# Kernel tuning notes

Measured on AMD Instinct MI355X. Metric: run time of the kernel, lower is better.

The kernel has to match this reference:

```python
import jax, jax.numpy as jnp
import numpy as np

DEPTH, HEADS, DIM_HEAD, DIM, MLP, PATCH_DIM, NP_, NC = 8, 8, 64, 512, 2048, 512, 1024, 2
INNER = HEADS * DIM_HEAD
SCALE = DIM_HEAD ** -0.5
EPS = 1e-5

def layernorm(x, s, b):
    m = x.mean(-1, keepdims=True)
    v = ((x - m) ** 2).mean(-1, keepdims=True)
    return (x - m) * jax.lax.rsqrt(v + EPS) * s + b

def setup_inputs() -> dict:
    key = jax.random.key(0)
    ks = jax.random.split(key, 24)
    g = lambda k, sh, sc=0.02: jax.random.normal(k, sh, dtype=jnp.float32) * sc
    return {
        "img": jax.random.normal(ks[0], (4, NP_, PATCH_DIM), dtype=jnp.float32),
        "embed_w": g(ks[1], (PATCH_DIM, DIM)), "embed_b": jnp.zeros((DIM,), jnp.float32),
        "pos_emb": g(ks[2], (1, NP_ + 1, DIM), 1.0), "cls_token": g(ks[3], (1, 1, DIM), 1.0),
        "ln1_s": jnp.ones((DEPTH, DIM), jnp.float32), "ln1_b": jnp.zeros((DEPTH, DIM), jnp.float32),
        "qkv_w": g(ks[4], (DEPTH, DIM, 3 * INNER)),
        "out_w": g(ks[5], (DEPTH, INNER, DIM)), "out_b": jnp.zeros((DEPTH, DIM), jnp.float32),
        "ln2_s": jnp.ones((DEPTH, DIM), jnp.float32), "ln2_b": jnp.zeros((DEPTH, DIM), jnp.float32),
        "ff_w1": g(ks[6], (DEPTH, DIM, MLP)), "ff_b1": jnp.zeros((DEPTH, MLP), jnp.float32),
        "ff_w2": g(ks[7], (DEPTH, MLP, DIM)), "ff_b2": jnp.zeros((DEPTH, DIM), jnp.float32),
        "head_ln_s": jnp.ones((DIM,), jnp.float32), "head_ln_b": jnp.zeros((DIM,), jnp.float32),
        "head_w": g(ks[8], (DIM, NC)), "head_b": jnp.zeros((NC,), jnp.float32),
    }

def reference(img, embed_w, embed_b, pos_emb, cls_token, ln1_s, ln1_b, qkv_w, out_w, out_b,
              ln2_s, ln2_b, ff_w1, ff_b1, ff_w2, ff_b2, head_ln_s, head_ln_b, head_w, head_b):
    B, N, _ = img.shape
    x = img @ embed_w + embed_b                       # [B, N, DIM]
    cls = jnp.broadcast_to(cls_token, (B, 1, DIM))
    x = jnp.concatenate([cls, x], axis=1) + pos_emb[:, :N + 1]
    for l in range(DEPTH):
        h = layernorm(x, ln1_s[l], ln1_b[l])
        qkv = h @ qkv_w[l]                            # [B, N+1, 3*INNER]
        q, k, v = jnp.split(qkv, 3, axis=-1)
        rh = lambda t: t.reshape(B, N + 1, HEADS, DIM_HEAD).transpose(0, 2, 1, 3)
        q, k, v = rh(q), rh(k), rh(v)                 # [B, H, N+1, Dh]
        dots = jnp.einsum('bhnd,bhmd->bhnm', q, k) * SCALE
        attn = jax.nn.softmax(dots, axis=-1)
        o = jnp.einsum('bhnm,bhmd->bhnd', attn, v)
        o = o.transpose(0, 2, 1, 3).reshape(B, N + 1, INNER)
        x = o @ out_w[l] + out_b[l] + x
        h = layernorm(x, ln2_s[l], ln2_b[l])
        h = jax.nn.gelu(h @ ff_w1[l] + ff_b1[l], approximate=False)
        x = h @ ff_w2[l] + ff_b2[l] + x
    x = x[:, 0]                                       # cls pooling
    x = layernorm(x, head_ln_s, head_ln_b)
    return (jax.nn.sigmoid(x @ head_w + head_b),)
```

## Files before the change

### kernel.cpp

```cpp
#include <hip/hip_runtime.h>
#include <math.h>
#include <stdint.h>

#define NHEADS   8
#define DHEAD    64
#define DIMM     512
#define MLPD     2048
#define NPATCH   1024
#define NTOK     1025
#define BATCH    4
#define ROWS     (BATCH*NTOK)
#define TOKPAD   1088
#define NCHUNK   17
#define CSPLIT   9
#define QSC      0.180336881f
#define LN_EPS   1e-5f

typedef __attribute__((ext_vector_type(8))) short short8;
typedef __attribute__((ext_vector_type(4))) float f32x4;

__device__ __forceinline__ unsigned short f2bf(float f) {
  union { float f; unsigned u; } c; c.f = f;
  unsigned u = c.u;
  return (unsigned short)((u + 0x7fffu + ((u >> 16) & 1u)) >> 16);
}
__device__ __forceinline__ unsigned short f2bf_fast(float f) {
  union { float f; unsigned u; } c; c.f = f;
  return (unsigned short)((c.u + 0x8000u) >> 16);
}
__device__ __forceinline__ float bf2f(unsigned short b) {
  union { unsigned u; float f; } c; c.u = (unsigned)b << 16;
  return c.f;
}

__device__ __forceinline__ float wsum(float v) {
#pragma unroll
  for (int o = 32; o > 0; o >>= 1) v += __shfl_xor(v, o, 64);
  return v;
}

__device__ __forceinline__ void gl_lds16(const void* g, const void* l) {
  __builtin_amdgcn_global_load_lds(
      (const __attribute__((address_space(1))) unsigned int*)(uintptr_t)g,
      (__attribute__((address_space(3))) unsigned int*)(unsigned int)(uintptr_t)l,
      16, 0, 0);
}

template <int TM, int TN, int WR, int WC, bool ACOMB>
__global__ __launch_bounds__(256) void mgemm_k(
    const unsigned short* __restrict__ A, const unsigned short* __restrict__ Bt,
    const float* __restrict__ bias, const float* __restrict__ res,
    void* __restrict__ Cout, int M, int N, int K, int flags,
    unsigned short* __restrict__ vTout, const float* __restrict__ mlc,
    const float* __restrict__ posp)
{
  constexpr int AF = TM / WR / 16;
  constexpr int BF = TN / WC / 16;
  constexpr int AG = TM / 32;
  constexpr int BG = TN / 32;
  __shared__ unsigned short sA[2][TM * 64];
  __shared__ unsigned short sB[2][TN * 64];
  const int tid = threadIdx.x;
  const int w = tid >> 6, lane = tid & 63;
  const int quad = lane >> 4, l15 = lane & 15;
  const int m0 = blockIdx.y * TM, n0 = blockIdx.x * TN;
  const int wrow = (w / WC) * (TM / WR);
  const int wcol = (w % WC) * (TN / WC);
  const int lrow = lane >> 3;
  const int lkg = (lane & 7) ^ lrow;

  size_t abase[AG], bbase[BG];
  int arow[AG];
#pragma unroll
  for (int g = 0; g < AG; g++) {
    int grp = w * AG + g;
    int ar = m0 + grp * 8 + lrow; ar = ar < M ? ar : M - 1;
    arow[g] = ar;
    abase[g] = (size_t)ar * K + lkg * 8;
  }
#pragma unroll
  for (int g = 0; g < BG; g++) {
    int grp = w * BG + g;
    int br = n0 + grp * 8 + lrow;
    bbase[g] = (size_t)br * K + lkg * 8;
  }

  auto stageB = [&](int k0, int buf) {
#pragma unroll
    for (int g = 0; g < BG; g++)
      gl_lds16(Bt + bbase[g] + k0, &sB[buf][(w * BG + g) * 512]);
  };
  auto stageA_dma = [&](int k0, int buf) {
#pragma unroll
    for (int g = 0; g < AG; g++)
      gl_lds16(A + abase[g] + k0, &sA[buf][(w * AG + g) * 512]);
  };

  uint4 ra0[AG], ra1[AG];
  float rl0[AG], rl1[AG];
  auto loadAC = [&](int k0) {
    const int h = k0 >> 6;
#pragma unroll
    for (int g = 0; g < AG; g++) {
      size_t off = abase[g] + k0;
      ra0[g] = *(const uint4*)(A + off);
      ra1[g] = *(const uint4*)(A + (size_t)ROWS * DIMM + off);
      int b = arow[g] / NTOK, tok = arow[g] - b * NTOK;
      int bh = b * 8 + h;
      rl0[g] = mlc[(size_t)bh * NTOK + tok];
      rl1[g] = mlc[(size_t)(32 + bh) * NTOK + tok];
    }
  };
  auto writeAC = [&](int buf) {
#pragma unroll
    for (int g = 0; g < AG; g++) {
      float inv = 1.0f / (rl0[g] + rl1[g]);
      const unsigned short* p0 = (const unsigned short*)&ra0[g];
      const unsigned short* p1 = (const unsigned short*)&ra1[g];
      alignas(16) unsigned short o[8];
#pragma unroll
      for (int i = 0; i < 8; i++)
        o[i] = f2bf((bf2f(p0[i]) + bf2f(p1[i])) * inv);
      *(uint4*)&sA[buf][(w * AG + g) * 512 + lane * 8] = *(const uint4*)o;
    }
  };

  f32x4 acc[AF][BF];
#pragma unroll
  for (int i = 0; i < AF; i++)
#pragma unroll
    for (int j = 0; j < BF; j++) { f32x4 z = {0.f, 0.f, 0.f, 0.f}; acc[i][j] = z; }

  if (ACOMB) { stageB(0, 0); loadAC(0); writeAC(0); }
  else       { stageA_dma(0, 0); stageB(0, 0); }

  const int nsteps = K >> 6;
  for (int step = 0; step < nsteps; step++) {
    const int buf = step & 1;
    __syncthreads();
    if (step + 1 < nsteps) {
      stageB((step + 1) << 6, buf ^ 1);
      if (ACOMB) loadAC((step + 1) << 6);
      else       stageA_dma((step + 1) << 6, buf ^ 1);
    }
#pragma unroll
    for (int kk = 0; kk < 2; kk++) {
      short8 af[AF], bfr[BF];
#pragma unroll
      for (int i = 0; i < AF; i++) {
        int r = wrow + i * 16 + l15;
        af[i] = *(const short8*)&sA[buf][r * 64 + (((kk * 4 + quad) ^ (lane & 7)) << 3)];
      }
#pragma unroll
      for (int j = 0; j < BF; j++) {
        int r = wcol + j * 16 + l15;
        bfr[j] = *(const short8*)&sB[buf][r * 64 + (((kk * 4 + quad) ^ (lane & 7)) << 3)];
      }
#pragma unroll
      for (int i = 0; i < AF; i++)
#pragma unroll
        for (int j = 0; j < BF; j++)
          acc[i][j] = __builtin_amdgcn_mfma_f32_16x16x32_bf16(af[i], bfr[j], acc[i][j], 0, 0, 0);
    }
    if (ACOMB && step + 1 < nsteps) writeAC(buf ^ 1);
  }

  const bool do_gelu = flags & 1;
  const bool out_bf  = flags & 2;
  const bool embedf  = flags & 4;
#pragma unroll
  for (int i = 0; i < AF; i++) {
#pragma unroll
    for (int j = 0; j < BF; j++) {
      const int col = n0 + wcol + j * 16 + l15;
      const bool vcol = (vTout != nullptr) && (col >= 1024);
      alignas(8) unsigned short vb[4];
#pragma unroll
      for (int rg = 0; rg < 4; rg++) {
        int row = m0 + wrow + i * 16 + quad * 4 + rg;
        if (row >= M) continue;
        float v = acc[i][j][rg];
        if (bias) v += bias[col];
        if (do_gelu) v = 0.5f * v * (1.0f + erff(v * 0.70710678118654752f));
        if (res) v += res[(size_t)row * N + col];
        if (embedf) {
          int bb = row >> 10, t = (row & 1023) + 1;
          ((float*)Cout)[((size_t)(bb * NTOK + t)) * N + col] =
              v + posp[(size_t)t * N + col];
        } else if (out_bf) {
          unsigned short bv = f2bf(v);
          vb[rg] = bv;
          if (!vcol) ((unsigned short*)Cout)[(size_t)row * N + col] = bv;
        } else {
          ((float*)Cout)[(size_t)row * N + col] = v;
        }
      }
      if (vcol) {
        const int hcol = col - 1024, h = hcol >> 6, d = hcol & 63;
#pragma unroll
        for (int rg = 0; rg < 4; rg++) {
          int row = m0 + wrow + i * 16 + quad * 4 + rg;
          if (row >= M) continue;
          int bb = row / NTOK, tok = row - bb * NTOK;
          vTout[((size_t)(bb * 8 + h) * 64 + d) * TOKPAD + tok] = vb[rg];
        }
      }
    }
  }
}

__global__ __launch_bounds__(256) void attn_k(
    const unsigned short* __restrict__ qkv, const unsigned short* __restrict__ vT,
    unsigned short* __restrict__ po, float* __restrict__ ml)
{
  __shared__ unsigned short ps[64 * 64];
  __shared__ unsigned short ks[2][64 * 64];
  __shared__ unsigned short vs[2][64 * 64];
  const int bid = blockIdx.x;
  const int g8 = bid & 7, ii = bid >> 3;
  const int bh = (g8 << 2) | (ii & 3);
  const int rest = ii >> 2;
  const int q0 = (rest % 17) * 64;
  const int split = rest / 17;
  const int b = bh >> 3, h = bh & 7;
  const int tid = threadIdx.x, w = tid >> 6, lane = tid & 63;
  const int quad = lane >> 4, l15 = lane & 15;
  const int lrow = lane >> 3, lkg = (lane & 7) ^ lrow;
  const unsigned short* qbase = qkv + (size_t)(b * NTOK) * 1536 + h * 64;
  const unsigned short* kbase = qbase + 512;
  const unsigned short* vtb   = vT + (size_t)bh * 64 * TOKPAD;

  auto stage_kv = [&](int c0, int buf) {
#pragma unroll
    for (int g = 0; g < 2; g++) {
      int grp = w * 2 + g;
      int tok = c0 + grp * 8 + lrow; tok = tok < NTOK ? tok : NTOK - 1;
      gl_lds16(kbase + (size_t)tok * 1536 + lkg * 8, &ks[buf][grp * 512]);
      int d = grp * 8 + lrow;
      gl_lds16(vtb + (size_t)d * TOKPAD + c0 + lkg * 8, &vs[buf][grp * 512]);
    }
  };

  const int cbeg = split ? CSPLIT : 0;
  const int cend = split ? NCHUNK : CSPLIT;
  stage_kv(cbeg * 64, 0);

  int qr = q0 + w * 16 + l15; qr = qr < NTOK ? qr : NTOK - 1;
  const unsigned short* qrow = qbase + (size_t)qr * 1536;
  short8 aq[2];
  aq[0] = *(const short8*)(qrow + quad * 8);
  aq[1] = *(const short8*)(qrow + 32 + quad * 8);
#pragma unroll
  for (int k = 0; k < 2; k++)
#pragma unroll
    for (int i = 0; i < 8; i++)
      aq[k][i] = (short)f2bf(bf2f((unsigned short)aq[k][i]) * QSC);

  short8 ones;
#pragma unroll
  for (int i = 0; i < 8; i++) ones[i] = (short)0x3F80;

  f32x4 Oa[4];
#pragma unroll
  for (int n = 0; n < 4; n++) { f32x4 z = {0.f, 0.f, 0.f, 0.f}; Oa[n] = z; }
  float lst[4] = {0.f, 0.f, 0.f, 0.f};

  for (int c = cbeg; c < cend; c++) {
    const int c0 = c * 64;
    const int buf = (c - cbeg) & 1;
    __syncthreads();
    if (c + 1 < cend) stage_kv(c0 + 64, buf ^ 1);

    f32x4 sa[4];
#pragma unroll
    for (int n = 0; n < 4; n++) {
      f32x4 s = {0.f, 0.f, 0.f, 0.f};
#pragma unroll
      for (int kk = 0; kk < 2; kk++) {
        short8 bk = *(const short8*)&ks[buf][(n * 16 + l15) * 64 + (((kk * 4 + quad) ^ (lane & 7)) << 3)];
        s = __builtin_amdgcn_mfma_f32_16x16x32_bf16(aq[kk], bk, s, 0, 0, 0);
      }
      sa[n] = s;
    }

    if (c0 + 64 > NTOK) {
#pragma unroll
      for (int n = 0; n < 4; n++) {
        bool oob = (c0 + n * 16 + l15) >= NTOK;
#pragma unroll
        for (int rg = 0; rg < 4; rg++)
          if (oob) sa[n][rg] = -1e30f;
      }
    }

#pragma unroll
    for (int n = 0; n < 4; n++)
#pragma unroll
      for (int rg = 0; rg < 4; rg++) {
        int row = w * 16 + quad * 4 + rg;
        int key = n * 16 + l15;
        ps[row * 64 + ((((key >> 3) ^ (row & 7)) & 7) << 3) + (key & 7)] =
            f2bf_fast(exp2f(sa[n][rg]));
      }

    short8 ap[2];
#pragma unroll
    for (int kk = 0; kk < 2; kk++)
      ap[kk] = *(const short8*)&ps[(w * 16 + l15) * 64 + (((kk * 4 + quad) ^ (lane & 7)) << 3)];

    f32x4 lsum = {0.f, 0.f, 0.f, 0.f};
#pragma unroll
    for (int kk = 0; kk < 2; kk++)
      lsum = __builtin_amdgcn_mfma_f32_16x16x32_bf16(ap[kk], ones, lsum, 0, 0, 0);
#pragma unroll
    for (int rg = 0; rg < 4; rg++) lst[rg] += lsum[rg];

#pragma unroll
    for (int n = 0; n < 4; n++) {
      f32x4 o = Oa[n];
#pragma unroll
      for (int kk = 0; kk < 2; kk++) {
        short8 bv = *(const short8*)&vs[buf][(n * 16 + l15) * 64 + (((kk * 4 + quad) ^ (lane & 7)) << 3)];
        o = __builtin_amdgcn_mfma_f32_16x16x32_bf16(ap[kk], bv, o, 0, 0, 0);
      }
      Oa[n] = o;
    }
  }

  unsigned short* pob = po + (size_t)split * ROWS * DIMM;
#pragma unroll
  for (int n = 0; n < 4; n++)
#pragma unroll
    for (int rg = 0; rg < 4; rg++) {
      int tok = q0 + w * 16 + quad * 4 + rg;
      if (tok < NTOK)
        pob[(size_t)(b * NTOK + tok) * DIMM + h * 64 + n * 16 + l15] = f2bf(Oa[n][rg]);
    }
  if (l15 == 0) {
#pragma unroll
    for (int rg = 0; rg < 4; rg++) {
      int tok = q0 + w * 16 + quad * 4 + rg;
      if (tok < NTOK)
        ml[(size_t)(split * 32 + bh) * NTOK + tok] = lst[rg];
    }
  }
}

__global__ __launch_bounds__(256) void ln_k(
    const float* __restrict__ X, const float* __restrict__ s,
    const float* __restrict__ b, unsigned short* __restrict__ Y, int nrows)
{
  const int w = threadIdx.x >> 6, lane = threadIdx.x & 63;
  const int row = blockIdx.x * 4 + w;
  if (row >= nrows) return;
  const float* x = X + (size_t)row * DIMM;
  float4 v0 = *(const float4*)(x + lane * 8);
  float4 v1 = *(const float4*)(x + lane * 8 + 4);
  float xv[8] = {v0.x, v0.y, v0.z, v0.w, v1.x, v1.y, v1.z, v1.w};
  float sum = 0.f, sq = 0.f;
#pragma unroll
  for (int i = 0; i < 8; i++) { sum += xv[i]; sq += xv[i] * xv[i]; }
  sum = wsum(sum); sq = wsum(sq);
  const float mean = sum * (1.0f / DIMM);
  const float var  = sq * (1.0f / DIMM) - mean * mean;
  const float r    = rsqrtf(var + LN_EPS);
  alignas(16) unsigned short tmp[8];
#pragma unroll
  for (int i = 0; i < 8; i++) {
    int d = lane * 8 + i;
    tmp[i] = f2bf((xv[i] - mean) * r * s[d] + b[d]);
  }
  *(uint4*)&Y[(size_t)row * DIMM + lane * 8] = *(const uint4*)tmp;
}

#define CLS_B   8
#define IMG_B   2048
#define TC0     (CLS_B + IMG_B)
#define TQKV    (TC0 + 64)
#define TOUT    (TQKV + 1536)
#define TFF1    (TOUT + 512)
#define TFF2    (TFF1 + 2048)
#define TEND    (TFF2 + 2048)

__global__ __launch_bounds__(256) void prep_k(
    const float* __restrict__ embed_w, const float* __restrict__ qkv_w,
    const float* __restrict__ out_w, const float* __restrict__ ff1_w,
    const float* __restrict__ ff2_w,
    unsigned short* __restrict__ wt_embed, unsigned short* __restrict__ wt_qkv,
    unsigned short* __restrict__ wt_out, unsigned short* __restrict__ wt_ff1,
    unsigned short* __restrict__ wt_ff2,
    const float* __restrict__ img, unsigned short* __restrict__ img_bf,
    const float* __restrict__ cls, const float* __restrict__ pos,
    float* __restrict__ x)
{
  __shared__ float tl[32][129];
  const int bid = blockIdx.x, tid = threadIdx.x;
  if (bid < CLS_B) {
    int idx = bid * 256 + tid;
    int b = idx >> 9, d = idx & 511;
    x[(size_t)b * NTOK * DIMM + d] = cls[d] + pos[d];
    return;
  }
  if (bid < TC0) {
    int i = (bid - CLS_B) * 256 + tid;
    float4 v = ((const float4*)img)[i];
    alignas(8) unsigned short o[4] = {f2bf(v.x), f2bf(v.y), f2bf(v.z), f2bf(v.w)};
    ((uint2*)img_bf)[i] = *(const uint2*)o;
    return;
  }
  const float* W; unsigned short* Wt; int K, N, t;
  if (bid < TQKV)      { W = embed_w; Wt = wt_embed; K = 512;  N = 512;  t = bid - TC0;  }
  else if (bid < TOUT) { W = qkv_w;   Wt = wt_qkv;   K = 512;  N = 1536; t = bid - TQKV; }
  else if (bid < TFF1) { W = out_w;   Wt = wt_out;   K = 512;  N = 512;  t = bid - TOUT; }
  else if (bid < TFF2) { W = ff1_w;   Wt = wt_ff1;   K = 512;  N = 2048; t = bid - TFF1; }
  else                 { W = ff2_w;   Wt = wt_ff2;   K = 2048; N = 512;  t = bid - TFF2; }
  const int ntx = N >> 5;
  const int tpz = ntx * (K >> 7);
  const int z = t / tpz, r = t - z * tpz;
  const int n0 = (r % ntx) << 5, k0 = (r / ntx) << 7;
  const size_t off = (size_t)z * K * N;
  const float* Wz = W + off;
  unsigned short* Wtz = Wt + off;
#pragma unroll
  for (int it = 0; it < 4; it++) {
    int lin = it * 256 + tid;
    int k = lin >> 3, f4 = (lin & 7) << 2;
    float4 v = *(const float4*)&Wz[(size_t)(k0 + k) * N + n0 + f4];
    tl[f4 + 0][k] = v.x; tl[f4 + 1][k] = v.y;
    tl[f4 + 2][k] = v.z; tl[f4 + 3][k] = v.w;
  }
  __syncthreads();
  const int n = tid >> 3, kg = tid & 7;
#pragma unroll
  for (int j = 0; j < 2; j++) {
    int kb = kg * 16 + j * 8;
    alignas(16) unsigned short o[8];
#pragma unroll
    for (int i = 0; i < 8; i++) o[i] = f2bf(tl[n][kb + i]);
    *(uint4*)&Wtz[(size_t)(n0 + n) * K + k0 + kb] = *(const uint4*)o;
  }
}

__global__ __launch_bounds__(256) void head_k(
    const float* __restrict__ X, const float* __restrict__ s,
    const float* __restrict__ bln, const float* __restrict__ W,
    const float* __restrict__ bh, float* __restrict__ out)
{
  const int w = threadIdx.x >> 6, lane = threadIdx.x & 63;
  if (w >= BATCH) return;
  const float* x = X + (size_t)w * NTOK * DIMM;
  float4 v0 = *(const float4*)(x + lane * 8);
  float4 v1 = *(const float4*)(x + lane * 8 + 4);
  float xv[8] = {v0.x, v0.y, v0.z, v0.w, v1.x, v1.y, v1.z, v1.w};
  float sum = 0.f, sq = 0.f;
#pragma unroll
  for (int i = 0; i < 8; i++) { sum += xv[i]; sq += xv[i] * xv[i]; }
  sum = wsum(sum); sq = wsum(sq);
  const float mean = sum * (1.0f / DIMM);
  const float var  = sq * (1.0f / DIMM) - mean * mean;
  const float r    = rsqrtf(var + LN_EPS);
  float l0 = 0.f, l1 = 0.f;
#pragma unroll
  for (int i = 0; i < 8; i++) {
    int d = lane * 8 + i;
    float xn = (xv[i] - mean) * r * s[d] + bln[d];
    l0 = fmaf(xn, W[d * 2 + 0], l0);
    l1 = fmaf(xn, W[d * 2 + 1], l1);
  }
  l0 = wsum(l0); l1 = wsum(l1);
  if (lane == 0) {
    out[w * 2 + 0] = 1.0f / (1.0f + expf(-(l0 + bh[0])));
    out[w * 2 + 1] = 1.0f / (1.0f + expf(-(l1 + bh[1])));
  }
}

extern "C" void kernel_launch(void* const* d_in, const int* in_sizes, int n_in,
                              void* d_out, int out_size, void* d_ws, size_t ws_size,
                              hipStream_t stream)
{
  const float* img       = (const float*)d_in[0];
  const float* embed_w   = (const float*)d_in[1];
  const float* embed_b   = (const float*)d_in[2];
  const float* pos_emb   = (const float*)d_in[3];
  const float* cls_token = (const float*)d_in[4];
  const float* ln1_s     = (const float*)d_in[5];
  const float* ln1_b     = (const float*)d_in[6];
  const float* qkv_w     = (const float*)d_in[7];
  const float* out_w     = (const float*)d_in[8];
  const float* out_b     = (const float*)d_in[9];
  const float* ln2_s     = (const float*)d_in[10];
  const float* ln2_b     = (const float*)d_in[11];
  const float* ff_w1     = (const float*)d_in[12];
  const float* ff_b1     = (const float*)d_in[13];
  const float* ff_w2     = (const float*)d_in[14];
  const float* ff_b2     = (const float*)d_in[15];
  const float* head_ln_s = (const float*)d_in[16];
  const float* head_ln_b = (const float*)d_in[17];
  const float* head_w    = (const float*)d_in[18];
  const float* head_b    = (const float*)d_in[19];
  float* out = (float*)d_out;

  char* p = (char*)d_ws;
  auto alloc = [&](size_t bytes) { char* r = p; p += (bytes + 255) & ~(size_t)255; return r; };

  unsigned short* wt_embed = (unsigned short*)alloc((size_t)512 * 512 * 2);
  unsigned short* wt_qkv   = (unsigned short*)alloc((size_t)8 * 1536 * 512 * 2);
  unsigned short* wt_out   = (unsigned short*)alloc((size_t)8 * 512 * 512 * 2);
  unsigned short* wt_ff1   = (unsigned short*)alloc((size_t)8 * 2048 * 512 * 2);
  unsigned short* wt_ff2   = (unsigned short*)alloc((size_t)8 * 512 * 2048 * 2);
  unsigned short* img_bf   = (unsigned short*)alloc((size_t)4096 * 512 * 2);
  float*          x        = (float*)alloc((size_t)ROWS * DIMM * 4);
  unsigned short* h        = (unsigned short*)alloc((size_t)ROWS * DIMM * 2);
  unsigned short* vTb      = (unsigned short*)alloc((size_t)32 * 64 * TOKPAD * 2);
  unsigned short* po       = (unsigned short*)alloc((size_t)2 * ROWS * DIMM * 2);
  float*          mlb      = (float*)alloc((size_t)2 * 32 * NTOK * 4);
  char*           big      = alloc((size_t)ROWS * MLPD * 2);
  unsigned short* qkvb     = (unsigned short*)big;
  unsigned short* ffh      = (unsigned short*)big;

  dim3 blk(256);

  prep_k<<<TEND, blk, 0, stream>>>(
      embed_w, qkv_w, out_w, ff_w1, ff_w2,
      wt_embed, wt_qkv, wt_out, wt_ff1, wt_ff2,
      img, img_bf, cls_token, pos_emb, x);

  mgemm_k<32, 64, 2, 2, false><<<dim3(8, 128), blk, 0, stream>>>(
      img_bf, wt_embed, embed_b, nullptr, x, 4096, 512, 512, 4,
      nullptr, nullptr, pos_emb);

  const int mt32 = (ROWS + 31) / 32;
  for (int l = 0; l < 8; l++) {
    ln_k<<<(ROWS + 3) / 4, blk, 0, stream>>>(
        x, ln1_s + l * DIMM, ln1_b + l * DIMM, h, ROWS);
    mgemm_k<32, 64, 2, 2, false><<<dim3(24, mt32), blk, 0, stream>>>(
        h, wt_qkv + (size_t)l * 1536 * 512, nullptr, nullptr,
        qkvb, ROWS, 1536, 512, 2, vTb, nullptr, nullptr);
    attn_k<<<dim3(1088), blk, 0, stream>>>(qkvb, vTb, po, mlb);
    mgemm_k<32, 64, 2, 2, true><<<dim3(8, mt32), blk, 0, stream>>>(
        po, wt_out + (size_t)l * 512 * 512, out_b + l * DIMM, x,
        x, ROWS, 512, 512, 0, nullptr, mlb, nullptr);
    ln_k<<<(ROWS + 3) / 4, blk, 0, stream>>>(
        x, ln2_s + l * DIMM, ln2_b + l * DIMM, h, ROWS);
    mgemm_k<32, 64, 2, 2, false><<<dim3(32, mt32), blk, 0, stream>>>(
        h, wt_ff1 + (size_t)l * 2048 * 512, ff_b1 + l * MLPD, nullptr,
        ffh, ROWS, 2048, 512, 1 | 2, nullptr, nullptr, nullptr);
    mgemm_k<32, 64, 2, 2, false><<<dim3(8, mt32), blk, 0, stream>>>(
        ffh, wt_ff2 + (size_t)l * 512 * 2048, ff_b2 + l * DIMM, x,
        x, ROWS, 512, 2048, 0, nullptr, nullptr, nullptr);
  }

  head_k<<<1, blk, 0, stream>>>(x, head_ln_s, head_ln_b, head_w, head_b, out);
}
```

Baseline: 1.190 ms.

## Process 128 query rows per attention block to reuse staged K/V tiles

Each attention block now covers 128 query rows instead of 64. Each wave handles two 16-row query groups against the same K/V chunk already staged in shared memory, and the grid shrinks from 1088 to 576 blocks. This halves the global-to-LDS K/V traffic and staging per query row. In exchange each wave holds twice as many accumulator registers, and there are fewer blocks to spread across the CUs, which may hurt occupancy and load balance.

```diff
diff --git a/kernel.cpp b/kernel.cpp
--- a/kernel.cpp
+++ b/kernel.cpp
@@ -220,8 +220,8 @@
   const int g8 = bid & 7, ii = bid >> 3;
   const int bh = (g8 << 2) | (ii & 3);
   const int rest = ii >> 2;
-  const int q0 = (rest % 17) * 64;
-  const int split = rest / 17;
+  const int q0 = (rest % 9) * 128;
+  const int split = rest / 9;
   const int b = bh >> 3, h = bh & 7;
   const int tid = threadIdx.x, w = tid >> 6, lane = tid & 63;
   const int quad = lane >> 4, l15 = lane & 15;
@@ -245,25 +245,30 @@
   const int cend = split ? NCHUNK : CSPLIT;
   stage_kv(cbeg * 64, 0);
 
-  int qr = q0 + w * 16 + l15; qr = qr < NTOK ? qr : NTOK - 1;
-  const unsigned short* qrow = qbase + (size_t)qr * 1536;
-  short8 aq[2];
-  aq[0] = *(const short8*)(qrow + quad * 8);
-  aq[1] = *(const short8*)(qrow + 32 + quad * 8);
-#pragma unroll
-  for (int k = 0; k < 2; k++)
-#pragma unroll
-    for (int i = 0; i < 8; i++)
-      aq[k][i] = (short)f2bf(bf2f((unsigned short)aq[k][i]) * QSC);
+  short8 aq[2][2];
+#pragma unroll
+  for (int g16 = 0; g16 < 2; g16++) {
+    int qr = q0 + w * 32 + g16 * 16 + l15; qr = qr < NTOK ? qr : NTOK - 1;
+    const unsigned short* qrow = qbase + (size_t)qr * 1536;
+    aq[g16][0] = *(const short8*)(qrow + quad * 8);
+    aq[g16][1] = *(const short8*)(qrow + 32 + quad * 8);
+#pragma unroll
+    for (int k = 0; k < 2; k++)
+#pragma unroll
+      for (int i = 0; i < 8; i++)
+        aq[g16][k][i] = (short)f2bf(bf2f((unsigned short)aq[g16][k][i]) * QSC);
+  }
 
   short8 ones;
 #pragma unroll
   for (int i = 0; i < 8; i++) ones[i] = (short)0x3F80;
 
-  f32x4 Oa[4];
-#pragma unroll
-  for (int n = 0; n < 4; n++) { f32x4 z = {0.f, 0.f, 0.f, 0.f}; Oa[n] = z; }
-  float lst[4] = {0.f, 0.f, 0.f, 0.f};
+  f32x4 Oa[2][4];
+#pragma unroll
+  for (int g16 = 0; g16 < 2; g16++)
+#pragma unroll
+    for (int n = 0; n < 4; n++) { f32x4 z = {0.f, 0.f, 0.f, 0.f}; Oa[g16][n] = z; }
+  float lst[2][4] = {{0.f, 0.f, 0.f, 0.f}, {0.f, 0.f, 0.f, 0.f}};
 
   for (int c = cbeg; c < cend; c++) {
     const int c0 = c * 64;
@@ -271,77 +276,83 @@
     __syncthreads();
     if (c + 1 < cend) stage_kv(c0 + 64, buf ^ 1);
 
-    f32x4 sa[4];
-#pragma unroll
-    for (int n = 0; n < 4; n++) {
-      f32x4 s = {0.f, 0.f, 0.f, 0.f};
-#pragma unroll
-      for (int kk = 0; kk < 2; kk++) {
-        short8 bk = *(const short8*)&ks[buf][(n * 16 + l15) * 64 + (((kk * 4 + quad) ^ (lane & 7)) << 3)];
-        s = __builtin_amdgcn_mfma_f32_16x16x32_bf16(aq[kk], bk, s, 0, 0, 0);
-      }
-      sa[n] = s;
-    }
-
-    if (c0 + 64 > NTOK) {
+#pragma unroll
+    for (int g16 = 0; g16 < 2; g16++) {
+      f32x4 sa[4];
 #pragma unroll
       for (int n = 0; n < 4; n++) {
-        bool oob = (c0 + n * 16 + l15) >= NTOK;
-#pragma unroll
-        for (int rg = 0; rg < 4; rg++)
-          if (oob) sa[n][rg] = -1e30f;
-      }
-    }
-
+        f32x4 s = {0.f, 0.f, 0.f, 0.f};
+#pragma unroll
+        for (int kk = 0; kk < 2; kk++) {
+          short8 bk = *(const short8*)&ks[buf][(n * 16 + l15) * 64 + (((kk * 4 + quad) ^ (lane & 7)) << 3)];
+          s = __builtin_amdgcn_mfma_f32_16x16x32_bf16(aq[g16][kk], bk, s, 0, 0, 0);
+        }
+        sa[n] = s;
+      }
+
+      if (c0 + 64 > NTOK) {
+#pragma unroll
+        for (int n = 0; n < 4; n++) {
+          bool oob = (c0 + n * 16 + l15) >= NTOK;
+#pragma unroll
+          for (int rg = 0; rg < 4; rg++)
+            if (oob) sa[n][rg] = -1e30f;
+        }
+      }
+
+#pragma unroll
+      for (int n = 0; n < 4; n++)
+#pragma unroll
+        for (int rg = 0; rg < 4; rg++) {
+          int row = w * 16 + quad * 4 + rg;
+          int key = n * 16 + l15;
+          ps[row * 64 + ((((key >> 3) ^ (row & 7)) & 7) << 3) + (key & 7)] =
+              f2bf_fast(exp2f(sa[n][rg]));
+        }
+
+      short8 ap[2];
+#pragma unroll
+      for (int kk = 0; kk < 2; kk++)
+        ap[kk] = *(const short8*)&ps[(w * 16 + l15) * 64 + (((kk * 4 + quad) ^ (lane & 7)) << 3)];
+
+      f32x4 lsum = {0.f, 0.f, 0.f, 0.f};
+#pragma unroll
+      for (int kk = 0; kk < 2; kk++)
+        lsum = __builtin_amdgcn_mfma_f32_16x16x32_bf16(ap[kk], ones, lsum, 0, 0, 0);
+#pragma unroll
+      for (int rg = 0; rg < 4; rg++) lst[g16][rg] += lsum[rg];
+
+#pragma unroll
+      for (int n = 0; n < 4; n++) {
+        f32x4 o = Oa[g16][n];
+#pragma unroll
+        for (int kk = 0; kk < 2; kk++) {
+          short8 bv = *(const short8*)&vs[buf][(n * 16 + l15) * 64 + (((kk * 4 + quad) ^ (lane & 7)) << 3)];
+          o = __builtin_amdgcn_mfma_f32_16x16x32_bf16(ap[kk], bv, o, 0, 0, 0);
+        }
+        Oa[g16][n] = o;
+      }
+    }
+  }
+
+  unsigned short* pob = po + (size_t)split * ROWS * DIMM;
+#pragma unroll
+  for (int g16 = 0; g16 < 2; g16++) {
 #pragma unroll
     for (int n = 0; n < 4; n++)
 #pragma unroll
       for (int rg = 0; rg < 4; rg++) {
-        int row = w * 16 + quad * 4 + rg;
-        int key = n * 16 + l15;
-        ps[row * 64 + ((((key >> 3) ^ (row & 7)) & 7) << 3) + (key & 7)] =
-            f2bf_fast(exp2f(sa[n][rg]));
-      }
-
-    short8 ap[2];
-#pragma unroll
-    for (int kk = 0; kk < 2; kk++)
-      ap[kk] = *(const short8*)&ps[(w * 16 + l15) * 64 + (((kk * 4 + quad) ^ (lane & 7)) << 3)];
-
-    f32x4 lsum = {0.f, 0.f, 0.f, 0.f};
-#pragma unroll
-    for (int kk = 0; kk < 2; kk++)
-      lsum = __builtin_amdgcn_mfma_f32_16x16x32_bf16(ap[kk], ones, lsum, 0, 0, 0);
-#pragma unroll
-    for (int rg = 0; rg < 4; rg++) lst[rg] += lsum[rg];
-
-#pragma unroll
-    for (int n = 0; n < 4; n++) {
-      f32x4 o = Oa[n];
-#pragma unroll
-      for (int kk = 0; kk < 2; kk++) {
-        short8 bv = *(const short8*)&vs[buf][(n * 16 + l15) * 64 + (((kk * 4 + quad) ^ (lane & 7)) << 3)];
-        o = __builtin_amdgcn_mfma_f32_16x16x32_bf16(ap[kk], bv, o, 0, 0, 0);
-      }
-      Oa[n] = o;
-    }
-  }
-
-  unsigned short* pob = po + (size_t)split * ROWS * DIMM;
-#pragma unroll
-  for (int n = 0; n < 4; n++)
-#pragma unroll
-    for (int rg = 0; rg < 4; rg++) {
-      int tok = q0 + w * 16 + quad * 4 + rg;
-      if (tok < NTOK)
-        pob[(size_t)(b * NTOK + tok) * DIMM + h * 64 + n * 16 + l15] = f2bf(Oa[n][rg]);
-    }
-  if (l15 == 0) {
-#pragma unroll
-    for (int rg = 0; rg < 4; rg++) {
-      int tok = q0 + w * 16 + quad * 4 + rg;
-      if (tok < NTOK)
-        ml[(size_t)(split * 32 + bh) * NTOK + tok] = lst[rg];
+        int tok = q0 + w * 32 + g16 * 16 + quad * 4 + rg;
+        if (tok < NTOK)
+          pob[(size_t)(b * NTOK + tok) * DIMM + h * 64 + n * 16 + l15] = f2bf(Oa[g16][n][rg]);
+      }
+    if (l15 == 0) {
+#pragma unroll
+      for (int rg = 0; rg < 4; rg++) {
+        int tok = q0 + w * 32 + g16 * 16 + quad * 4 + rg;
+        if (tok < NTOK)
+          ml[(size_t)(split * 32 + bh) * NTOK + tok] = lst[g16][rg];
+      }
     }
   }
 }
@@ -536,7 +547,7 @@
     mgemm_k<32, 64, 2, 2, false><<<dim3(24, mt32), blk, 0, stream>>>(
         h, wt_qkv + (size_t)l * 1536 * 512, nullptr, nullptr,
         qkvb, ROWS, 1536, 512, 2, vTb, nullptr, nullptr);
-    attn_k<<<dim3(1088), blk, 0, stream>>>(qkvb, vTb, po, mlb);
+    attn_k<<<dim3(576), blk, 0, stream>>>(qkvb, vTb, po, mlb);
     mgemm_k<32, 64, 2, 2, true><<<dim3(8, mt32), blk, 0, stream>>>(
         po, wt_out + (size_t)l * 512 * 512, out_b + l * DIMM, x,
         x, ROWS, 512, 512, 0, nullptr, mlb, nullptr);
```

Result: slower. 1.222 ms (+2.7%).
